# Kernel optimization log

Hardware: AMD Instinct MI355X
Metric: run time of the kernel (lower is better)

## Reference

```python
import jax, jax.numpy as jnp
import numpy as np

N_NODES = 50000
N_EDGES = 800000
IN_F, HID, OUT_F = 128, 128, 64


def setup_inputs() -> dict:
    key = jax.random.key(0)
    k1, k2, k3, k4 = jax.random.split(key, 4)
    x = jax.random.normal(k1, (N_NODES, IN_F), dtype=jnp.float32)
    edge_index = jax.random.randint(k2, (2, N_EDGES), 0, N_NODES, dtype=jnp.int64)
    # Glorot-style scaled weights, zero bias (PyG GCNConv default)
    W1 = jax.random.normal(k3, (IN_F, HID), dtype=jnp.float32) * (1.0 / np.sqrt(IN_F))
    b1 = jnp.zeros((HID,), dtype=jnp.float32)
    W2 = jax.random.normal(k4, (HID, OUT_F), dtype=jnp.float32) * (1.0 / np.sqrt(HID))
    b2 = jnp.zeros((OUT_F,), dtype=jnp.float32)
    return {"x": x, "edge_index": edge_index, "W1": W1, "b1": b1, "W2": W2, "b2": b2}


def reference(x, edge_index, W1, b1, W2, b2):
    n = x.shape[0]
    # add self-loops (PyG GCNConv default add_self_loops=True)
    loop = jnp.arange(n, dtype=edge_index.dtype)
    src = jnp.concatenate([edge_index[0], loop])  # message source nodes
    dst = jnp.concatenate([edge_index[1], loop])  # aggregation target nodes
    # symmetric normalization: D^{-1/2} (A+I) D^{-1/2}
    deg = jax.ops.segment_sum(jnp.ones(dst.shape, dtype=x.dtype), dst, num_segments=n)
    dinv = jnp.where(deg > 0, jax.lax.rsqrt(deg), 0.0)
    norm = dinv[src] * dinv[dst]  # [E+N]

    def gcn_conv(h, W, b):
        h = h @ W                              # dense transform first (PyG order)
        msg = h[src] * norm[:, None]           # gather + scale: [E+N, d]
        agg = jax.ops.segment_sum(msg, dst, num_segments=n)  # scatter-add
        return agg + b

    h = jax.nn.relu(gcn_conv(x, W1, b1))
    return gcn_conv(h, W2, b2)
```

## Files before the change

### kernel.cpp

```cpp
#include <hip/hip_runtime.h>
#include <hip/hip_bf16.h>

#define NN   50000
#define NE   800000
#define F_IN 128
#define F_H  128
#define F_O  64

#define BINSHIFT 7
#define NBINS    ((NN + 127) >> 7)
#define CAP      2816
#define EPB      2048

static constexpr int NB_NODE = (NN + 255) / 256;
static constexpr int NB_G1   = (NN + 63) / 64;

typedef __bf16 bf16_8 __attribute__((ext_vector_type(8)));
typedef float  f32x4  __attribute__((ext_vector_type(4)));

template <typename AT, int K, int NOUT, bool SCALE>
__device__ __forceinline__ void gemm_body(const AT* __restrict__ X,
                                          const float* __restrict__ W,
                                          const float* __restrict__ dinv,
                                          __hip_bfloat16* __restrict__ Y,
                                          __hip_bfloat16* WB, int blk) {
    constexpr int NKS = K / 32;
    constexpr int NC  = NOUT / 16;
    const int t = threadIdx.x;
    for (int f = t; f < K * NOUT; f += 256) {
        int k = f / NOUT, n = f % NOUT;
        int ks = k >> 5, kr = k & 31, qq = kr >> 3, jj = kr & 7;
        int c = n >> 4, nn = n & 15;
        WB[(((ks * NC + c) * 16 + nn) * 4 + qq) * 8 + jj] = __float2bfloat16(W[f]);
    }
    __syncthreads();

    const int wave = t >> 6, lane = t & 63;
    const int r = lane & 15, q = lane >> 4;
    const int m0 = blk * 64 + wave * 16;
    int arow = m0 + r;
    if (arow >= NN) arow = NN - 1;

    f32x4 acc[NC];
#pragma unroll
    for (int c = 0; c < NC; ++c) acc[c] = (f32x4){0.f, 0.f, 0.f, 0.f};

#pragma unroll
    for (int ks = 0; ks < NKS; ++ks) {
        bf16_8 a;
        if constexpr (sizeof(AT) == 4) {
            const float* xp = (const float*)X + (size_t)arow * K + ks * 32 + q * 8;
            float4 x0 = ((const float4*)xp)[0];
            float4 x1 = ((const float4*)xp)[1];
            a[0] = (__bf16)x0.x; a[1] = (__bf16)x0.y; a[2] = (__bf16)x0.z; a[3] = (__bf16)x0.w;
            a[4] = (__bf16)x1.x; a[5] = (__bf16)x1.y; a[6] = (__bf16)x1.z; a[7] = (__bf16)x1.w;
        } else {
            a = *(const bf16_8*)((const __hip_bfloat16*)X + (size_t)arow * K + ks * 32 + q * 8);
        }
#pragma unroll
        for (int c = 0; c < NC; ++c) {
            bf16_8 b = *(const bf16_8*)&WB[(((ks * NC + c) * 16 + r) * 4 + q) * 8];
            acc[c] = __builtin_amdgcn_mfma_f32_16x16x32_bf16(a, b, acc[c], 0, 0, 0);
        }
    }

#pragma unroll
    for (int c = 0; c < NC; ++c) {
#pragma unroll
        for (int i = 0; i < 4; ++i) {
            int gr = m0 + q * 4 + i;
            if (gr < NN) {
                float v = acc[c][i];
                if constexpr (SCALE) v *= dinv[gr];
                Y[(size_t)gr * NOUT + c * 16 + r] = __float2bfloat16(v);
            }
        }
    }
}

__global__ __launch_bounds__(256) void k_fuseA(const float* __restrict__ X,
                                               const float* __restrict__ W1,
                                               __hip_bfloat16* __restrict__ Xw,
                                               const int* __restrict__ ei32,
                                               int2* __restrict__ binbuf,
                                               unsigned* __restrict__ bincnt) {
    __shared__ __align__(16) char smem[32768];
    const int t = threadIdx.x;

    if (blockIdx.x < NB_G1) {
        gemm_body<float, F_IN, F_H, false>(X, W1, nullptr, Xw,
                                           (__hip_bfloat16*)smem, blockIdx.x);
        return;
    }

    unsigned* hist = (unsigned*)smem;
    unsigned* base = hist + NBINS;
    unsigned* rank = base + NBINS;
    for (int i = t; i < NBINS; i += 256) { hist[i] = 0u; rank[i] = 0u; }
    __syncthreads();

    const bool is64 = ((ei32[1] | ei32[3] | ei32[5] | ei32[7]) == 0);
    const int e0 = (blockIdx.x - NB_G1) * EPB;
    int es[8], ed[8];
#pragma unroll
    for (int j = 0; j < 8; ++j) {
        int e = e0 + t + j * 256;
        if (e < NE) {
            if (is64) {
                const long long* p = (const long long*)ei32;
                es[j] = (int)p[e];
                ed[j] = (int)p[NE + e];
            } else {
                es[j] = ei32[e];
                ed[j] = ei32[NE + e];
            }
        } else ed[j] = -1;
    }
#pragma unroll
    for (int j = 0; j < 8; ++j)
        if (ed[j] >= 0) atomicAdd(&hist[ed[j] >> BINSHIFT], 1u);
    __syncthreads();
    for (int b = t; b < NBINS; b += 256)
        base[b] = atomicAdd(&bincnt[b], hist[b]);
    __syncthreads();
#pragma unroll
    for (int j = 0; j < 8; ++j) {
        if (ed[j] >= 0) {
            int b = ed[j] >> BINSHIFT;
            unsigned rk = atomicAdd(&rank[b], 1u);
            binbuf[(size_t)b * CAP + base[b] + rk] = make_int2(es[j], ed[j]);
        }
    }
}

__global__ __launch_bounds__(256) void k_bincount(const int2* __restrict__ binbuf,
                                                  const unsigned* __restrict__ bincnt,
                                                  unsigned* __restrict__ cnt) {
    __shared__ unsigned h[128];
    const int b = blockIdx.x;
    if (threadIdx.x < 128) h[threadIdx.x] = 0u;
    __syncthreads();
    const unsigned n = bincnt[b];
    for (unsigned i = threadIdx.x; i < n; i += 256)
        atomicAdd(&h[binbuf[(size_t)b * CAP + i].y & 127], 1u);
    __syncthreads();
    int node = (b << BINSHIFT) + threadIdx.x;
    if (threadIdx.x < 128 && node < NN) cnt[node] = h[threadIdx.x];
}

__global__ __launch_bounds__(256) void k_blocksum(const unsigned* __restrict__ cnt,
                                                  unsigned* __restrict__ bsum) {
    __shared__ unsigned s[256];
    int i = blockIdx.x * 256 + threadIdx.x;
    unsigned v = (i < NN) ? cnt[i] : 0u;
    s[threadIdx.x] = v;
    __syncthreads();
    for (int off = 128; off > 0; off >>= 1) {
        if (threadIdx.x < off) s[threadIdx.x] += s[threadIdx.x + off];
        __syncthreads();
    }
    if (threadIdx.x == 0) bsum[blockIdx.x] = s[0];
}

__global__ __launch_bounds__(256) void k_scan_bsums(const unsigned* __restrict__ bsum,
                                                    unsigned* __restrict__ bscan) {
    __shared__ unsigned s[256];
    unsigned v = (threadIdx.x < NB_NODE) ? bsum[threadIdx.x] : 0u;
    s[threadIdx.x] = v;
    __syncthreads();
    for (int off = 1; off < 256; off <<= 1) {
        unsigned t = (threadIdx.x >= (unsigned)off) ? s[threadIdx.x - off] : 0u;
        __syncthreads();
        s[threadIdx.x] += t;
        __syncthreads();
    }
    if (threadIdx.x < NB_NODE) bscan[threadIdx.x] = s[threadIdx.x] - v;
}

__global__ __launch_bounds__(256) void k_scan_local(const unsigned* __restrict__ cnt,
                                                    const unsigned* __restrict__ bscan,
                                                    unsigned* __restrict__ row_ptr,
                                                    float* __restrict__ dinv) {
    __shared__ unsigned s[256];
    int i = blockIdx.x * 256 + threadIdx.x;
    unsigned v = (i < NN) ? cnt[i] : 0u;
    s[threadIdx.x] = v;
    __syncthreads();
    for (int off = 1; off < 256; off <<= 1) {
        unsigned t = (threadIdx.x >= (unsigned)off) ? s[threadIdx.x - off] : 0u;
        __syncthreads();
        s[threadIdx.x] += t;
        __syncthreads();
    }
    if (i < NN) {
        row_ptr[i] = bscan[blockIdx.x] + s[threadIdx.x] - v;
        dinv[i]    = 1.0f / sqrtf((float)(v + 1u));
    }
    if (i == 0) row_ptr[NN] = NE;
}

__global__ __launch_bounds__(256) void k_phaseB(const int2* __restrict__ binbuf,
                                                const unsigned* __restrict__ bincnt,
                                                const unsigned* __restrict__ row_ptr,
                                                int* __restrict__ srcs) {
    __shared__ unsigned lcur[128];
    const int b = blockIdx.x;
    const int node0 = b << BINSHIFT;
    if (threadIdx.x < 128) {
        int node = node0 + threadIdx.x;
        lcur[threadIdx.x] = (node < NN) ? row_ptr[node] : 0u;
    }
    __syncthreads();
    const unsigned n = bincnt[b];
    for (unsigned i = threadIdx.x; i < n; i += 256) {
        int2 p = binbuf[(size_t)b * CAP + i];
        unsigned pos = atomicAdd(&lcur[p.y & 127], 1u);
        srcs[pos] = p.x;
    }
}

__global__ __launch_bounds__(256) void k_agg1(const __hip_bfloat16* __restrict__ Xw,
                                              const int* __restrict__ srcs,
                                              const unsigned* __restrict__ row_ptr,
                                              const float* __restrict__ dinv,
                                              const float* __restrict__ b1,
                                              __hip_bfloat16* __restrict__ H) {
    int wv   = (blockIdx.x * 256 + threadIdx.x) >> 6;
    int lane = threadIdx.x & 63;
    if (wv >= NN) return;
    const __hip_bfloat162* X2 = (const __hip_bfloat162*)Xw;
    const float dn = dinv[wv];
    float2 self = __bfloat1622float2(X2[(size_t)wv * 64 + lane]);
    float2 ac0 = make_float2(dn * self.x, dn * self.y);
    float2 ac1 = make_float2(0.f, 0.f);
    unsigned i  = row_ptr[wv];
    unsigned ie = row_ptr[wv + 1];
    for (; i + 3 < ie; i += 4) {
        int s0 = srcs[i], s1 = srcs[i + 1], s2 = srcs[i + 2], s3 = srcs[i + 3];
        float d0 = dinv[s0], d1 = dinv[s1], d2 = dinv[s2], d3 = dinv[s3];
        float2 v0 = __bfloat1622float2(X2[(size_t)s0 * 64 + lane]);
        float2 v1 = __bfloat1622float2(X2[(size_t)s1 * 64 + lane]);
        float2 v2 = __bfloat1622float2(X2[(size_t)s2 * 64 + lane]);
        float2 v3 = __bfloat1622float2(X2[(size_t)s3 * 64 + lane]);
        ac0.x += d0 * v0.x; ac0.y += d0 * v0.y;
        ac1.x += d1 * v1.x; ac1.y += d1 * v1.y;
        ac0.x += d2 * v2.x; ac0.y += d2 * v2.y;
        ac1.x += d3 * v3.x; ac1.y += d3 * v3.y;
    }
    for (; i < ie; ++i) {
        int s = srcs[i];
        float d = dinv[s];
        float2 v = __bfloat1622float2(X2[(size_t)s * 64 + lane]);
        ac0.x += d * v.x; ac0.y += d * v.y;
    }
    float o0 = fmaxf(dn * (ac0.x + ac1.x) + b1[2 * lane], 0.f);
    float o1 = fmaxf(dn * (ac0.y + ac1.y) + b1[2 * lane + 1], 0.f);
    ((__hip_bfloat162*)H)[(size_t)wv * 64 + lane] = __float22bfloat162_rn(make_float2(o0, o1));
}

__global__ __launch_bounds__(256) void k_gemm2(const __hip_bfloat16* __restrict__ H1,
                                               const float* __restrict__ W2,
                                               const float* __restrict__ dinv,
                                               __hip_bfloat16* __restrict__ Hw) {
    __shared__ __align__(16) __hip_bfloat16 WB[(F_H / 32) * (F_O / 16) * 512];
    gemm_body<__hip_bfloat16, F_H, F_O, true>(H1, W2, dinv, Hw, WB, blockIdx.x);
}

__global__ __launch_bounds__(256) void k_agg2(const __hip_bfloat16* __restrict__ Hw,
                                              const int* __restrict__ srcs,
                                              const unsigned* __restrict__ row_ptr,
                                              const float* __restrict__ dinv,
                                              const float* __restrict__ b2,
                                              float* __restrict__ out) {
    int wv   = (blockIdx.x * 256 + threadIdx.x) >> 6;
    int lane = threadIdx.x & 63;
    if (wv >= NN) return;
    float ac0 = __bfloat162float(Hw[(size_t)wv * 64 + lane]);
    float ac1 = 0.f;
    unsigned i  = row_ptr[wv];
    unsigned ie = row_ptr[wv + 1];
    for (; i + 3 < ie; i += 4) {
        int s0 = srcs[i], s1 = srcs[i + 1], s2 = srcs[i + 2], s3 = srcs[i + 3];
        float v0 = __bfloat162float(Hw[(size_t)s0 * 64 + lane]);
        float v1 = __bfloat162float(Hw[(size_t)s1 * 64 + lane]);
        float v2 = __bfloat162float(Hw[(size_t)s2 * 64 + lane]);
        float v3 = __bfloat162float(Hw[(size_t)s3 * 64 + lane]);
        ac0 += v0 + v2;
        ac1 += v1 + v3;
    }
    for (; i < ie; ++i) ac0 += __bfloat162float(Hw[(size_t)srcs[i] * 64 + lane]);
    out[(size_t)wv * 64 + lane] = dinv[wv] * (ac0 + ac1) + b2[lane];
}

extern "C" void kernel_launch(void* const* d_in, const int* in_sizes, int n_in,
                              void* d_out, int out_size, void* d_ws, size_t ws_size,
                              hipStream_t stream) {
    const float* x  = (const float*)d_in[0];
    const int*   ei = (const int*)d_in[1];
    const float* W1 = (const float*)d_in[2];
    const float* b1 = (const float*)d_in[3];
    const float* W2 = (const float*)d_in[4];
    const float* b2 = (const float*)d_in[5];
    float* out = (float*)d_out;

    char* w = (char*)d_ws;
    size_t off = 0;
    auto alloc = [&](size_t bytes) {
        void* p = w + off;
        off += (bytes + 255) & ~(size_t)255;
        return p;
    };
    unsigned* cnt     = (unsigned*)alloc((size_t)NN * 4);
    unsigned* row_ptr = (unsigned*)alloc((size_t)(NN + 1) * 4);
    float*    dinv    = (float*)alloc((size_t)NN * 4);
    unsigned* bsum    = (unsigned*)alloc(256 * 4);
    unsigned* bscan   = (unsigned*)alloc(256 * 4);
    unsigned* bincnt  = (unsigned*)alloc((size_t)NBINS * 4);
    int*      srcs    = (int*)alloc((size_t)NE * 4);
    int2*     binbuf  = (int2*)alloc((size_t)NBINS * CAP * 8);
    __hip_bfloat16* Xw = (__hip_bfloat16*)alloc((size_t)NN * F_H * 2);
    __hip_bfloat16* H1 = (__hip_bfloat16*)alloc((size_t)NN * F_H * 2);
    __hip_bfloat16* Hw = Xw;

    const int NB_BIN = (NE + EPB - 1) / EPB;

    hipMemsetAsync(bincnt, 0, (size_t)NBINS * 4, stream);
    k_fuseA<<<NB_G1 + NB_BIN, 256, 0, stream>>>(x, W1, Xw, ei, binbuf, bincnt);
    k_bincount<<<NBINS, 256, 0, stream>>>(binbuf, bincnt, cnt);
    k_blocksum<<<NB_NODE, 256, 0, stream>>>(cnt, bsum);
    k_scan_bsums<<<1, 256, 0, stream>>>(bsum, bscan);
    k_scan_local<<<NB_NODE, 256, 0, stream>>>(cnt, bscan, row_ptr, dinv);
    k_phaseB<<<NBINS, 256, 0, stream>>>(binbuf, bincnt, row_ptr, srcs);

    k_agg1<<<(NN + 3) / 4, 256, 0, stream>>>(Xw, srcs, row_ptr, dinv, b1, H1);
    k_gemm2<<<(NN + 63) / 64, 256, 0, stream>>>(H1, W2, dinv, Hw);
    k_agg2<<<(NN + 3) / 4, 256, 0, stream>>>(Hw, srcs, row_ptr, dinv, b2, out);
}
```

Before: 209.1 us.

## Pack edges into one int, fuse CSR build kernels, vectorize aggregation gathers

Edges are binned as one packed int (source shifted left, low 7 bits of destination), which halves the bin buffer traffic. The per-node count, block sum, scan and scatter kernels collapse into a single-block scan over bin totals plus one phase kernel that builds a local prefix sum, writes row_ptr and dinv, and scatters sources. That removes three launches and their global round trips. Both aggregation kernels now load 16-byte bf16x8 rows and split the edges across lane subgroups, combining partial sums with xor shuffles; this relies on source ids fitting in 25 bits.

Measured after the change: 192.5 us. 1.09x faster.

```diff
diff --git a/kernel.cpp b/kernel.cpp
--- a/kernel.cpp
+++ b/kernel.cpp
@@ -12,8 +12,7 @@
 #define CAP      2816
 #define EPB      2048
 
-static constexpr int NB_NODE = (NN + 255) / 256;
-static constexpr int NB_G1   = (NN + 63) / 64;
+static constexpr int NB_G1 = (NN + 63) / 64;
 
 typedef __bf16 bf16_8 __attribute__((ext_vector_type(8)));
 typedef float  f32x4  __attribute__((ext_vector_type(4)));
@@ -82,7 +81,7 @@
                                                const float* __restrict__ W1,
                                                __hip_bfloat16* __restrict__ Xw,
                                                const int* __restrict__ ei32,
-                                               int2* __restrict__ binbuf,
+                                               int* __restrict__ binbuf,
                                                unsigned* __restrict__ bincnt) {
     __shared__ __align__(16) char smem[32768];
     const int t = threadIdx.x;
@@ -101,121 +100,95 @@
 
     const bool is64 = ((ei32[1] | ei32[3] | ei32[5] | ei32[7]) == 0);
     const int e0 = (blockIdx.x - NB_G1) * EPB;
-    int es[8], ed[8];
+    int pk[8], bin[8];
 #pragma unroll
     for (int j = 0; j < 8; ++j) {
         int e = e0 + t + j * 256;
         if (e < NE) {
+            int s, d;
             if (is64) {
                 const long long* p = (const long long*)ei32;
-                es[j] = (int)p[e];
-                ed[j] = (int)p[NE + e];
+                s = (int)p[e];
+                d = (int)p[NE + e];
             } else {
-                es[j] = ei32[e];
-                ed[j] = ei32[NE + e];
+                s = ei32[e];
+                d = ei32[NE + e];
             }
-        } else ed[j] = -1;
+            pk[j]  = (s << BINSHIFT) | (d & 127);
+            bin[j] = d >> BINSHIFT;
+        } else bin[j] = -1;
     }
 #pragma unroll
     for (int j = 0; j < 8; ++j)
-        if (ed[j] >= 0) atomicAdd(&hist[ed[j] >> BINSHIFT], 1u);
+        if (bin[j] >= 0) atomicAdd(&hist[bin[j]], 1u);
     __syncthreads();
     for (int b = t; b < NBINS; b += 256)
         base[b] = atomicAdd(&bincnt[b], hist[b]);
     __syncthreads();
 #pragma unroll
     for (int j = 0; j < 8; ++j) {
-        if (ed[j] >= 0) {
-            int b = ed[j] >> BINSHIFT;
-            unsigned rk = atomicAdd(&rank[b], 1u);
-            binbuf[(size_t)b * CAP + base[b] + rk] = make_int2(es[j], ed[j]);
-        }
-    }
-}
-
-__global__ __launch_bounds__(256) void k_bincount(const int2* __restrict__ binbuf,
-                                                  const unsigned* __restrict__ bincnt,
-                                                  unsigned* __restrict__ cnt) {
+        if (bin[j] >= 0) {
+            unsigned rk = atomicAdd(&rank[bin[j]], 1u);
+            binbuf[(size_t)bin[j] * CAP + base[bin[j]] + rk] = pk[j];
+        }
+    }
+}
+
+__global__ __launch_bounds__(512) void k_binscan(const unsigned* __restrict__ bincnt,
+                                                 unsigned* __restrict__ bscan) {
+    __shared__ unsigned s[512];
+    const int t = threadIdx.x;
+    unsigned v = (t < NBINS) ? bincnt[t] : 0u;
+    s[t] = v;
+    __syncthreads();
+    for (int off = 1; off < 512; off <<= 1) {
+        unsigned u = (t >= off) ? s[t - off] : 0u;
+        __syncthreads();
+        s[t] += u;
+        __syncthreads();
+    }
+    if (t < NBINS) bscan[t] = s[t] - v;
+}
+
+__global__ __launch_bounds__(256) void k_phaseB(const int* __restrict__ binbuf,
+                                                const unsigned* __restrict__ bincnt,
+                                                const unsigned* __restrict__ bscan,
+                                                unsigned* __restrict__ row_ptr,
+                                                float* __restrict__ dinv,
+                                                int* __restrict__ srcs) {
     __shared__ unsigned h[128];
-    const int b = blockIdx.x;
-    if (threadIdx.x < 128) h[threadIdx.x] = 0u;
+    __shared__ unsigned cur[128];
+    const int b = blockIdx.x, t = threadIdx.x;
+    if (t < 128) h[t] = 0u;
     __syncthreads();
     const unsigned n = bincnt[b];
-    for (unsigned i = threadIdx.x; i < n; i += 256)
-        atomicAdd(&h[binbuf[(size_t)b * CAP + i].y & 127], 1u);
-    __syncthreads();
-    int node = (b << BINSHIFT) + threadIdx.x;
-    if (threadIdx.x < 128 && node < NN) cnt[node] = h[threadIdx.x];
-}
-
-__global__ __launch_bounds__(256) void k_blocksum(const unsigned* __restrict__ cnt,
-                                                  unsigned* __restrict__ bsum) {
-    __shared__ unsigned s[256];
-    int i = blockIdx.x * 256 + threadIdx.x;
-    unsigned v = (i < NN) ? cnt[i] : 0u;
-    s[threadIdx.x] = v;
-    __syncthreads();
-    for (int off = 128; off > 0; off >>= 1) {
-        if (threadIdx.x < off) s[threadIdx.x] += s[threadIdx.x + off];
+    const int* buf = binbuf + (size_t)b * CAP;
+    for (unsigned i = t; i < n; i += 256)
+        atomicAdd(&h[buf[i] & 127], 1u);
+    __syncthreads();
+    if (t < 128) cur[t] = h[t];
+    __syncthreads();
+    for (int off = 1; off < 128; off <<= 1) {
+        unsigned u = (t < 128 && t >= off) ? cur[t - off] : 0u;
         __syncthreads();
-    }
-    if (threadIdx.x == 0) bsum[blockIdx.x] = s[0];
-}
-
-__global__ __launch_bounds__(256) void k_scan_bsums(const unsigned* __restrict__ bsum,
-                                                    unsigned* __restrict__ bscan) {
-    __shared__ unsigned s[256];
-    unsigned v = (threadIdx.x < NB_NODE) ? bsum[threadIdx.x] : 0u;
-    s[threadIdx.x] = v;
-    __syncthreads();
-    for (int off = 1; off < 256; off <<= 1) {
-        unsigned t = (threadIdx.x >= (unsigned)off) ? s[threadIdx.x - off] : 0u;
+        if (t < 128) cur[t] += u;
         __syncthreads();
-        s[threadIdx.x] += t;
-        __syncthreads();
-    }
-    if (threadIdx.x < NB_NODE) bscan[threadIdx.x] = s[threadIdx.x] - v;
-}
-
-__global__ __launch_bounds__(256) void k_scan_local(const unsigned* __restrict__ cnt,
-                                                    const unsigned* __restrict__ bscan,
-                                                    unsigned* __restrict__ row_ptr,
-                                                    float* __restrict__ dinv) {
-    __shared__ unsigned s[256];
-    int i = blockIdx.x * 256 + threadIdx.x;
-    unsigned v = (i < NN) ? cnt[i] : 0u;
-    s[threadIdx.x] = v;
-    __syncthreads();
-    for (int off = 1; off < 256; off <<= 1) {
-        unsigned t = (threadIdx.x >= (unsigned)off) ? s[threadIdx.x - off] : 0u;
-        __syncthreads();
-        s[threadIdx.x] += t;
-        __syncthreads();
-    }
-    if (i < NN) {
-        row_ptr[i] = bscan[blockIdx.x] + s[threadIdx.x] - v;
-        dinv[i]    = 1.0f / sqrtf((float)(v + 1u));
-    }
-    if (i == 0) row_ptr[NN] = NE;
-}
-
-__global__ __launch_bounds__(256) void k_phaseB(const int2* __restrict__ binbuf,
-                                                const unsigned* __restrict__ bincnt,
-                                                const unsigned* __restrict__ row_ptr,
-                                                int* __restrict__ srcs) {
-    __shared__ unsigned lcur[128];
-    const int b = blockIdx.x;
-    const int node0 = b << BINSHIFT;
-    if (threadIdx.x < 128) {
-        int node = node0 + threadIdx.x;
-        lcur[threadIdx.x] = (node < NN) ? row_ptr[node] : 0u;
-    }
-    __syncthreads();
-    const unsigned n = bincnt[b];
-    for (unsigned i = threadIdx.x; i < n; i += 256) {
-        int2 p = binbuf[(size_t)b * CAP + i];
-        unsigned pos = atomicAdd(&lcur[p.y & 127], 1u);
-        srcs[pos] = p.x;
+    }
+    if (t < 128) {
+        unsigned ex = bscan[b] + cur[t] - h[t];
+        int node = (b << BINSHIFT) + t;
+        if (node < NN) {
+            row_ptr[node] = ex;
+            dinv[node]    = rsqrtf((float)(h[t] + 1u));
+        }
+        cur[t] = ex;
+    }
+    if (b == NBINS - 1 && t == 0) row_ptr[NN] = NE;
+    __syncthreads();
+    for (unsigned i = t; i < n; i += 256) {
+        int p = buf[i];
+        unsigned pos = atomicAdd(&cur[p & 127], 1u);
+        srcs[pos] = p >> BINSHIFT;
     }
 }
 
@@ -225,37 +198,41 @@
                                               const float* __restrict__ dinv,
                                               const float* __restrict__ b1,
                                               __hip_bfloat16* __restrict__ H) {
-    int wv   = (blockIdx.x * 256 + threadIdx.x) >> 6;
-    int lane = threadIdx.x & 63;
+    const int wv   = (blockIdx.x * 256 + threadIdx.x) >> 6;
+    const int lane = threadIdx.x & 63;
     if (wv >= NN) return;
-    const __hip_bfloat162* X2 = (const __hip_bfloat162*)Xw;
+    const int sub = lane >> 4;
+    const int fl  = lane & 15;
     const float dn = dinv[wv];
-    float2 self = __bfloat1622float2(X2[(size_t)wv * 64 + lane]);
-    float2 ac0 = make_float2(dn * self.x, dn * self.y);
-    float2 ac1 = make_float2(0.f, 0.f);
-    unsigned i  = row_ptr[wv];
-    unsigned ie = row_ptr[wv + 1];
-    for (; i + 3 < ie; i += 4) {
-        int s0 = srcs[i], s1 = srcs[i + 1], s2 = srcs[i + 2], s3 = srcs[i + 3];
-        float d0 = dinv[s0], d1 = dinv[s1], d2 = dinv[s2], d3 = dinv[s3];
-        float2 v0 = __bfloat1622float2(X2[(size_t)s0 * 64 + lane]);
-        float2 v1 = __bfloat1622float2(X2[(size_t)s1 * 64 + lane]);
-        float2 v2 = __bfloat1622float2(X2[(size_t)s2 * 64 + lane]);
-        float2 v3 = __bfloat1622float2(X2[(size_t)s3 * 64 + lane]);
-        ac0.x += d0 * v0.x; ac0.y += d0 * v0.y;
-        ac1.x += d1 * v1.x; ac1.y += d1 * v1.y;
-        ac0.x += d2 * v2.x; ac0.y += d2 * v2.y;
-        ac1.x += d3 * v3.x; ac1.y += d3 * v3.y;
-    }
-    for (; i < ie; ++i) {
+
+    float acc[8];
+    bf16_8 self = *(const bf16_8*)(Xw + (size_t)wv * F_H + fl * 8);
+    const float sw = (sub == 0) ? dn : 0.f;
+#pragma unroll
+    for (int j = 0; j < 8; ++j) acc[j] = sw * (float)self[j];
+
+    const unsigned ie = row_ptr[wv + 1];
+    for (unsigned i = row_ptr[wv] + sub; i < ie; i += 4) {
         int s = srcs[i];
-        float d = dinv[s];
-        float2 v = __bfloat1622float2(X2[(size_t)s * 64 + lane]);
-        ac0.x += d * v.x; ac0.y += d * v.y;
-    }
-    float o0 = fmaxf(dn * (ac0.x + ac1.x) + b1[2 * lane], 0.f);
-    float o1 = fmaxf(dn * (ac0.y + ac1.y) + b1[2 * lane + 1], 0.f);
-    ((__hip_bfloat162*)H)[(size_t)wv * 64 + lane] = __float22bfloat162_rn(make_float2(o0, o1));
+        float dsc = dinv[s];
+        bf16_8 row = *(const bf16_8*)(Xw + (size_t)s * F_H + fl * 8);
+#pragma unroll
+        for (int j = 0; j < 8; ++j) acc[j] += dsc * (float)row[j];
+    }
+#pragma unroll
+    for (int j = 0; j < 8; ++j) {
+        acc[j] += __shfl_xor(acc[j], 16, 64);
+        acc[j] += __shfl_xor(acc[j], 32, 64);
+    }
+    if (sub == 0) {
+        bf16_8 o;
+#pragma unroll
+        for (int j = 0; j < 8; ++j) {
+            float v = fmaxf(dn * acc[j] + b1[fl * 8 + j], 0.f);
+            o[j] = (__bf16)v;
+        }
+        *(bf16_8*)(H + (size_t)wv * F_H + fl * 8) = o;
+    }
 }
 
 __global__ __launch_bounds__(256) void k_gemm2(const __hip_bfloat16* __restrict__ H1,
@@ -272,24 +249,40 @@
                                               const float* __restrict__ dinv,
                                               const float* __restrict__ b2,
                                               float* __restrict__ out) {
-    int wv   = (blockIdx.x * 256 + threadIdx.x) >> 6;
-    int lane = threadIdx.x & 63;
+    const int wv   = (blockIdx.x * 256 + threadIdx.x) >> 6;
+    const int lane = threadIdx.x & 63;
     if (wv >= NN) return;
-    float ac0 = __bfloat162float(Hw[(size_t)wv * 64 + lane]);
-    float ac1 = 0.f;
-    unsigned i  = row_ptr[wv];
-    unsigned ie = row_ptr[wv + 1];
-    for (; i + 3 < ie; i += 4) {
-        int s0 = srcs[i], s1 = srcs[i + 1], s2 = srcs[i + 2], s3 = srcs[i + 3];
-        float v0 = __bfloat162float(Hw[(size_t)s0 * 64 + lane]);
-        float v1 = __bfloat162float(Hw[(size_t)s1 * 64 + lane]);
-        float v2 = __bfloat162float(Hw[(size_t)s2 * 64 + lane]);
-        float v3 = __bfloat162float(Hw[(size_t)s3 * 64 + lane]);
-        ac0 += v0 + v2;
-        ac1 += v1 + v3;
-    }
-    for (; i < ie; ++i) ac0 += __bfloat162float(Hw[(size_t)srcs[i] * 64 + lane]);
-    out[(size_t)wv * 64 + lane] = dinv[wv] * (ac0 + ac1) + b2[lane];
+    const int sub = lane >> 3;
+    const int fl  = lane & 7;
+
+    float acc[8];
+    bf16_8 self = *(const bf16_8*)(Hw + (size_t)wv * F_O + fl * 8);
+#pragma unroll
+    for (int j = 0; j < 8; ++j) acc[j] = (sub == 0) ? (float)self[j] : 0.f;
+
+    const unsigned ie = row_ptr[wv + 1];
+    for (unsigned i = row_ptr[wv] + sub; i < ie; i += 8) {
+        int s = srcs[i];
+        bf16_8 row = *(const bf16_8*)(Hw + (size_t)s * F_O + fl * 8);
+#pragma unroll
+        for (int j = 0; j < 8; ++j) acc[j] += (float)row[j];
+    }
+#pragma unroll
+    for (int j = 0; j < 8; ++j) {
+        acc[j] += __shfl_xor(acc[j], 8, 64);
+        acc[j] += __shfl_xor(acc[j], 16, 64);
+        acc[j] += __shfl_xor(acc[j], 32, 64);
+    }
+    if (sub == 0) {
+        float dn = dinv[wv];
+        float4 o0 = make_float4(dn * acc[0] + b2[fl * 8 + 0], dn * acc[1] + b2[fl * 8 + 1],
+                                dn * acc[2] + b2[fl * 8 + 2], dn * acc[3] + b2[fl * 8 + 3]);
+        float4 o1 = make_float4(dn * acc[4] + b2[fl * 8 + 4], dn * acc[5] + b2[fl * 8 + 5],
+                                dn * acc[6] + b2[fl * 8 + 6], dn * acc[7] + b2[fl * 8 + 7]);
+        float4* op = (float4*)(out + (size_t)wv * F_O + fl * 8);
+        op[0] = o0;
+        op[1] = o1;
+    }
 }
 
 extern "C" void kernel_launch(void* const* d_in, const int* in_sizes, int n_in,
@@ -310,14 +303,12 @@
         off += (bytes + 255) & ~(size_t)255;
         return p;
     };
-    unsigned* cnt     = (unsigned*)alloc((size_t)NN * 4);
     unsigned* row_ptr = (unsigned*)alloc((size_t)(NN + 1) * 4);
     float*    dinv    = (float*)alloc((size_t)NN * 4);
-    unsigned* bsum    = (unsigned*)alloc(256 * 4);
-    unsigned* bscan   = (unsigned*)alloc(256 * 4);
     unsigned* bincnt  = (unsigned*)alloc((size_t)NBINS * 4);
+    unsigned* bscan   = (unsigned*)alloc((size_t)NBINS * 4);
     int*      srcs    = (int*)alloc((size_t)NE * 4);
-    int2*     binbuf  = (int2*)alloc((size_t)NBINS * CAP * 8);
+    int*      binbuf  = (int*)alloc((size_t)NBINS * CAP * 4);
     __hip_bfloat16* Xw = (__hip_bfloat16*)alloc((size_t)NN * F_H * 2);
     __hip_bfloat16* H1 = (__hip_bfloat16*)alloc((size_t)NN * F_H * 2);
     __hip_bfloat16* Hw = Xw;
@@ -326,11 +317,8 @@
 
     hipMemsetAsync(bincnt, 0, (size_t)NBINS * 4, stream);
     k_fuseA<<<NB_G1 + NB_BIN, 256, 0, stream>>>(x, W1, Xw, ei, binbuf, bincnt);
-    k_bincount<<<NBINS, 256, 0, stream>>>(binbuf, bincnt, cnt);
-    k_blocksum<<<NB_NODE, 256, 0, stream>>>(cnt, bsum);
-    k_scan_bsums<<<1, 256, 0, stream>>>(bsum, bscan);
-    k_scan_local<<<NB_NODE, 256, 0, stream>>>(cnt, bscan, row_ptr, dinv);
-    k_phaseB<<<NBINS, 256, 0, stream>>>(binbuf, bincnt, row_ptr, srcs);
+    k_binscan<<<1, 512, 0, stream>>>(bincnt, bscan);
+    k_phaseB<<<NBINS, 256, 0, stream>>>(binbuf, bincnt, bscan, row_ptr, dinv, srcs);
 
     k_agg1<<<(NN + 3) / 4, 256, 0, stream>>>(Xw, srcs, row_ptr, dinv, b1, H1);
     k_gemm2<<<(NN + 63) / 64, 256, 0, stream>>>(H1, W2, dinv, Hw);
```
